# Kernel tuning notes

Measured on AMD Instinct MI355X. Metric: run time of the kernel, lower is better.

## Reference

```python
import jax, jax.numpy as jnp
import numpy as np

B, T, D = 16, 2048, 512
DB, K, TOPK, WIN = 128, 7, 16, 64
GATE_CAP = 0.5
STRAND_CAP = 0.5
_PHI = 1.618033988749895
_PSI = -0.6180339887498949


def _ln(x, w, b):
    mu = jnp.mean(x, -1, keepdims=True)
    var = jnp.var(x, -1, keepdims=True)
    return (x - mu) * jax.lax.rsqrt(var + 1e-5) * w + b


def setup_inputs() -> dict:
    key = jax.random.key(0)
    ks = jax.random.split(key, 20)
    def nrm(i, shape, scale=1.0):
        return jax.random.normal(ks[i], shape, dtype=jnp.float32) * jnp.float32(scale)
    return {
        'X_write': nrm(0, (B, T, D)),
        'X_read': nrm(1, (B, T, D)),
        'slots': nrm(2, (B, K, DB)),
        'W0': nrm(3, (D, D), D ** -0.5),
        'ln_write_w': jnp.ones((D,), jnp.float32),
        'ln_write_b': jnp.zeros((D,), jnp.float32),
        'W_V': nrm(4, (D, DB), D ** -0.5),
        'W_K_slot': nrm(5, (DB, DB), DB ** -0.5),
        'slot_key_bias': nrm(6, (K, DB), 2.0),
        'W_gate_w': nrm(7, (2 * DB, DB), (2 * DB) ** -0.5),
        'W_gate_b': jnp.full((DB,), -2.0, jnp.float32),
        'ln_strand_w': jnp.ones((DB,), jnp.float32),
        'ln_strand_b': jnp.zeros((DB,), jnp.float32),
        'Ws_Q': nrm(8, (DB, DB), DB ** -0.5),
        'Ws_K': nrm(9, (DB, DB), DB ** -0.5),
        'Ws_V': nrm(10, (DB, DB), DB ** -0.5),
        'lambda_strand': nrm(11, (DB,), 0.5),
        'W_Q_read': nrm(12, (D, DB), D ** -0.5),
        'W_K_read': nrm(13, (DB, DB), DB ** -0.5),
        'W_V_read': nrm(14, (DB, D), DB ** -0.5),
        'render_coeffs': nrm(15, (K, 3, D), 0.2),
        'slot_temps': jnp.ones((K,), jnp.float32),
    }


def _forward(X_write, X_read, slots, W0, ln_write_w, ln_write_b, W_V, W_K_slot,
             slot_key_bias, W_gate_w, W_gate_b, ln_strand_w, ln_strand_b,
             Ws_Q, Ws_K, Ws_V, lambda_strand, W_Q_read, W_K_read, W_V_read,
             render_coeffs, slot_temps):
    scale = jnp.float32(DB ** -0.5)
    W0_sg = jax.lax.stop_gradient(W0)
    X_n = _ln(X_write, ln_write_w, ln_write_b)

    # ---- windowed salience + topk pair selection (no-grad in original) ----
    X_nsg = jax.lax.stop_gradient(X_n)
    X_W0 = X_nsg @ W0_sg.T                      # [B,T,D]
    NEG = jnp.float32(-1e30)
    sal = []
    for o in range(1, WIN + 1):                 # offset j = i - o, fixed small loop
        s = jnp.sum(X_nsg[:, o:, :] * X_W0[:, :-o, :], axis=-1)  # [B, T-o]
        sal.append(jnp.pad(s, ((0, 0), (o, 0)), constant_values=NEG))
    sal = jnp.stack(sal, axis=-1).reshape(B, T * WIN)
    _, flat_idx = jax.lax.top_k(sal, TOPK)      # [B, TOPK]
    i_idx = flat_idx // WIN
    j_idx = i_idx - (flat_idx % WIN + 1)

    # ---- gather pairs, salience-weighted relation vector ----
    x_newer = jnp.take_along_axis(X_n, i_idx[:, :, None], axis=1)   # [B,TOPK,D]
    x_older = jnp.take_along_axis(X_n, j_idx[:, :, None], axis=1)
    pair_sal = jnp.sum(x_newer * (x_older @ W0_sg.T), axis=-1)      # [B,TOPK]
    alpha = jax.nn.softmax(pair_sal, axis=-1)
    rel = (x_newer - x_older) @ W_V                                 # [B,TOPK,DB]
    R_t = jnp.einsum('bk,bkd->bd', alpha, rel)                      # [B,DB]

    # ---- gated slot write ----
    slot_keys = slots @ W_K_slot + slot_key_bias                    # [B,K,DB]
    compat = jnp.einsum('bkd,bd->bk', slot_keys, R_t) * scale * jax.nn.softplus(slot_temps)
    sw = jax.nn.softmax(compat, axis=-1)
    weighted_R = sw[:, :, None] * R_t[:, None, :]                   # [B,K,DB]
    g = jax.nn.sigmoid(jnp.concatenate([slots, weighted_R], -1) @ W_gate_w + W_gate_b)
    slots_upd = (1.0 - g) * slots + g * weighted_R

    # ---- K x K strand mixer ----
    Bn = _ln(slots_upd, ln_strand_w, ln_strand_b)
    sa = jax.nn.softmax(jnp.einsum('bqd,bkd->bqk', Bn @ Ws_Q, Bn @ Ws_K) * scale, axis=-1)
    ctx = sa @ (Bn @ Ws_V)
    slots_next = slots_upd + ctx * jnp.clip(jnp.tanh(lambda_strand), -STRAND_CAP, STRAND_CAP)

    # ---- aux losses ----
    L_persist = jnp.mean((slots_next - slots) ** 2)
    nrm = jnp.maximum(jnp.linalg.norm(slots_next, axis=-1, keepdims=True), 1e-12)
    Bnorm = slots_next / nrm
    cos = jnp.einsum('bkd,bjd->bkj', Bnorm, Bnorm)
    off = ~jnp.eye(K, dtype=bool)
    L_div = jnp.mean((cos ** 2)[:, off])

    # ---- directional gated read attention ----
    q_r = X_read @ W_Q_read                                         # [B,T,DB]
    k_r = slots_next @ W_K_read                                     # [B,K,DB]
    v_r = slots_next @ W_V_read                                     # [B,K,D]
    scores = jnp.einsum('btd,bkd->btk', q_r, k_r) * scale
    q_mean = jnp.mean(X_read, axis=1)                               # [B,D]
    w0q = q_mean @ W0_sg.T
    denom = jnp.float32(_PHI - _PSI)
    phi_q = (w0q - _PSI * q_mean) / denom
    psi_q = (_PHI * q_mean - w0q) / denom
    phi_mag = jnp.linalg.norm(phi_q, axis=-1, keepdims=True)
    psi_mag = jnp.linalg.norm(psi_q, axis=-1, keepdims=True)
    total = phi_mag + psi_mag + 1e-6
    basis = jnp.concatenate([jnp.ones_like(phi_mag), phi_mag / total, psi_mag / total], -1)  # [B,3]
    gate = jnp.clip(jnp.tanh(jnp.einsum('bi,kid->bkd', basis, render_coeffs)), -GATE_CAP, GATE_CAP)
    z = jnp.einsum('btk,bkd->btd', jax.nn.softmax(scores, axis=-1), v_r * gate)
    return z, slots_next, L_persist, L_div


def reference(X_write, X_read, slots, W0, ln_write_w, ln_write_b, W_V, W_K_slot,
              slot_key_bias, W_gate_w, W_gate_b, ln_strand_w, ln_strand_b,
              Ws_Q, Ws_K, Ws_V, lambda_strand, W_Q_read, W_K_read, W_V_read,
              render_coeffs, slot_temps):
    return _forward(X_write, X_read, slots, W0, ln_write_w, ln_write_b, W_V, W_K_slot,
                    slot_key_bias, W_gate_w, W_gate_b, ln_strand_w, ln_strand_b,
                    Ws_Q, Ws_K, Ws_V, lambda_strand, W_Q_read, W_K_read, W_V_read,
                    render_coeffs, slot_temps)
```

## Files before the change

kernel.cpp:

```cpp
#include <hip/hip_runtime.h>
#include <math.h>

#define B_ 16
#define T_ 2048
#define D_ 512
#define DB_ 128
#define K_ 7
#define TOPK_ 16
#define WIN_ 64

static constexpr float SCALE_ = 0.08838834764831845f;
static constexpr float PHI_ = 1.618033988749895f;
static constexpr float PSI_ = -0.6180339887498949f;
static constexpr float INV_DENOM_ = 0.4472135954999579f;
static constexpr float NEGV = -1e30f;
static constexpr float NEGINF = -3.402823466e38f;
#define IMAXI 0x7FFFFFFF

typedef __attribute__((ext_vector_type(8))) __bf16 bf16x8;
typedef __attribute__((ext_vector_type(8))) unsigned short u16x8;
typedef __attribute__((ext_vector_type(4))) float f32x4;

__device__ inline float softplusf(float x){
    return fmaxf(x, 0.f) + log1pf(expf(-fabsf(x)));
// ... 84 lines not shown
        unsigned short h0 = f2bf(v.x), h1 = f2bf(v.y), h2 = f2bf(v.z), h3 = f2bf(v.w);
        ushort4 hv = make_ushort4(h0, h1, h2, h3);
        ushort4 lv = make_ushort4(f2bf(v.x - bf2f(h0)), f2bf(v.y - bf2f(h1)),
                                  f2bf(v.z - bf2f(h2)), f2bf(v.w - bf2f(h3)));
        *(ushort4*)&Wh[(size_t)gid*4] = hv;
        *(ushort4*)&Wl[(size_t)gid*4] = lv;
    } else {
        int idx = bx - 4352;
        int b_ = idx >> 5, c = idx & 31;
        const float* base = Xr + ((size_t)(b_*T_ + c*64)) * D_;
        float s0 = 0.f, s1 = 0.f;
        for (int t = 0; t < 64; t++) {
            s0 += base[(size_t)t*D_ + tid];
            s1 += base[(size_t)t*D_ + tid + 256];
        }
        qpart[((size_t)b_*32 + c)*D_ + tid] = s0;
        qpart[((size_t)b_*32 + c)*D_ + tid + 256] = s1;
    }
}

__global__ __launch_bounds__(256) void gemm_xw0_mfma(const unsigned short* __restrict__ Ah,
                                                     const unsigned short* __restrict__ Al,
                                                     const unsigned short* __restrict__ Wh,
                                                     const unsigned short* __restrict__ Wl,
                                                     float* __restrict__ Cf)
{
    __shared__ __align__(16) unsigned short sAh[2*128*32], sAl[2*128*32], sBh[2*128*32], sBl[2*128*32];
    int t0 = blockIdx.x * 128, d0 = blockIdx.y * 128;
    int tid = threadIdx.x;
    int lane = tid & 63, wid = tid >> 6;
    int wr = wid >> 1, wc = wid & 1;
    int fr = lane & 15;
    int kc2 = ((((lane >> 4) + (fr >> 1)) & 3) * 8);

    f32x4 acc[4][4];
    #pragma unroll
    for (int m = 0; m < 4; m++)
        #pragma unroll
        for (int n = 0; n < 4; n++) acc[m][n] = (f32x4){0.f,0.f,0.f,0.f};

    const unsigned short* gs = (wid==0) ? Ah : (wid==1) ? Al : (wid==2) ? Wh : Wl;
    unsigned short* lsA = (wid==0) ? sAh : (wid==1) ? sAl : (wid==2) ? sBh : sBl;
    int rowoff = (wid < 2) ? t0 : d0;
    int cch = ((lane & 3) - ((lane >> 3) & 3)) & 3;
    const unsigned short* gbase = gs + (size_t)(rowoff + (lane >> 2))*512 + cch*8;

    #pragma unroll
    for (int i = 0; i < 8; i++)
        gload16(gbase + (size_t)(16*i)*512 + 0, lsA + i*512);

    for (int t = 0; t < 16; t++) {
        int cur = t & 1;
        __syncthreads();
        if (t < 15) {
            unsigned short* ls = lsA + (cur^1)*(128*32);
            int kk = (t+1)*32;
            #pragma unroll
            for (int i = 0; i < 8; i++)
                gload16(gbase + (size_t)(16*i)*512 + kk, ls + i*512);
        }
        int bo = cur*(128*32);
        bf16x8 ahf[4], alf[4], bhf[4], blf[4];
        #pragma unroll
        for (int m = 0; m < 4; m++) {
            int r = bo + (wr*64 + m*16 + fr)*32 + kc2;
            ahf[m] = ld_bf8(&sAh[r]);
            alf[m] = ld_bf8(&sAl[r]);
        }
        #pragma unroll
        for (int n = 0; n < 4; n++) {
            int r = bo + (wc*64 + n*16 + fr)*32 + kc2;
            bhf[n] = ld_bf8(&sBh[r]);
            blf[n] = ld_bf8(&sBl[r]);
        }
        #pragma unroll
        for (int m = 0; m < 4; m++)
            #pragma unroll
            for (int n = 0; n < 4; n++) {
                acc[m][n] = __builtin_amdgcn_mfma_f32_16x16x32_bf16(bhf[n], ahf[m], acc[m][n], 0, 0, 0);
                acc[m][n] = __builtin_amdgcn_mfma_f32_16x16x32_bf16(bhf[n], alf[m], acc[m][n], 0, 0, 0);
                acc[m][n] = __builtin_amdgcn_mfma_f32_16x16x32_bf16(blf[n], ahf[m], acc[m][n], 0, 0, 0);
            }
    }

    #pragma unroll
    for (int m = 0; m < 4; m++) {
        int t = t0 + wr*64 + m*16 + fr;
        #pragma unroll
        for (int n = 0; n < 4; n++) {
            int dbase = d0 + wc*64 + n*16 + (lane >> 4)*4;
            *(f32x4*)&Cf[(size_t)t*512 + dbase] = acc[m][n];
        }
    }
}

__global__ __launch_bounds__(256) void sal_mfma(const unsigned short* __restrict__ Xh,
                                                const unsigned short* __restrict__ Xl,
                                                const float* __restrict__ Cf,
                                                float* __restrict__ sal)
{
    int b = blockIdx.x, i0 = blockIdx.y * 64;
    __shared__ __align__(16) unsigned short sAh[64*32], sAl[64*32], sBh[128*32], sBl[128*32];
    int tid = threadIdx.x;
    int lane = tid & 63, wcw = tid >> 6;
    int fr = lane & 15;
    int kc2 = ((((lane >> 4) + (fr >> 1)) & 3) * 8);

    const unsigned short* XhB = Xh + (size_t)b*T_*D_;
    const unsigned short* XlB = Xl + (size_t)b*T_*D_;
    const float* CfB = Cf + (size_t)b*T_*D_;

    f32x4 acc[4][2];
    #pragma unroll
    for (int m = 0; m < 4; m++) { acc[m][0] = (f32x4){0.f,0.f,0.f,0.f}; acc[m][1] = (f32x4){0.f,0.f,0.f,0.f}; }

    int ar = tid >> 2, ac = tid & 3;
    int aslot = (ac + (ar >> 1)) & 3;
    int brow = tid >> 1, bhh = tid & 1;
    int jrow = i0 - 64 + brow;

    uint4 rAh, rAl;
    float4 rB0[2], rB1[2];

    auto LOAD = [&](int kk){
        rAh = *(const uint4*)(XhB + (size_t)(i0 + ar)*512 + kk + ac*8);
        rAl = *(const uint4*)(XlB + (size_t)(i0 + ar)*512 + kk + ac*8);
        #pragma unroll
        for (int cc = 0; cc < 2; cc++) {
            int c = 2*bhh + cc;
            if (jrow >= 0) {
                const float* src = CfB + (size_t)jrow*512 + kk + c*8;
                rB0[cc] = *(const float4*)src;
                rB1[cc] = *(const float4*)(src + 4);
            } else {
                rB0[cc] = make_float4(0.f,0.f,0.f,0.f);
                rB1[cc] = make_float4(0.f,0.f,0.f,0.f);
            }
        }
    };
    auto WRITE = [&](){
        *(uint4*)&sAh[ar*32 + aslot*8] = rAh;
        *(uint4*)&sAl[ar*32 + aslot*8] = rAl;
        #pragma unroll
        for (int cc = 0; cc < 2; cc++) {
            int c = 2*bhh + cc;
            int slot = (c + (brow >> 1)) & 3;
            uint4 hv, lv;
            float4 v0 = rB0[cc], v1 = rB1[cc];
            unsigned int h01 = pkbf(v0.x, v0.y), h23 = pkbf(v0.z, v0.w);
            unsigned int h45 = pkbf(v1.x, v1.y), h67 = pkbf(v1.z, v1.w);
            float r0 = v0.x - __uint_as_float(h01 << 16);
            float r1 = v0.y - __uint_as_float(h01 & 0xFFFF0000u);
            float r2 = v0.z - __uint_as_float(h23 << 16);
            float r3 = v0.w - __uint_as_float(h23 & 0xFFFF0000u);
            float r4 = v1.x - __uint_as_float(h45 << 16);
            float r5 = v1.y - __uint_as_float(h45 & 0xFFFF0000u);
            float r6 = v1.z - __uint_as_float(h67 << 16);
            float r7 = v1.w - __uint_as_float(h67 & 0xFFFF0000u);
            hv.x = h01; hv.y = h23; hv.z = h45; hv.w = h67;
            lv.x = pkbf(r0, r1); lv.y = pkbf(r2, r3); lv.z = pkbf(r4, r5); lv.w = pkbf(r6, r7);
            *(uint4*)&sBh[brow*32 + slot*8] = hv;
            *(uint4*)&sBl[brow*32 + slot*8] = lv;
        }
    };

    LOAD(0);
    for (int t = 0; t < 16; t++) {
        WRITE();
        __syncthreads();
        int kkn = (t+1)*32;
        bf16x8 ahf[4], alf[4], bhf[2], blf[2];
        #pragma unroll
        for (int m = 0; m < 4; m++) {
            int r = (m*16 + fr)*32 + kc2;
            ahf[m] = ld_bf8(&sAh[r]);
            alf[m] = ld_bf8(&sAl[r]);
        }
        #pragma unroll
        for (int n = 0; n < 2; n++) {
            int r = (wcw*32 + n*16 + fr)*32 + kc2;
            bhf[n] = ld_bf8(&sBh[r]);
            blf[n] = ld_bf8(&sBl[r]);
        }
        if (t < 15) LOAD(kkn);
        #pragma unroll
        for (int m = 0; m < 4; m++)
            #pragma unroll
            for (int n = 0; n < 2; n++) {
                acc[m][n] = __builtin_amdgcn_mfma_f32_16x16x32_bf16(ahf[m], bhf[n], acc[m][n], 0, 0, 0);
                acc[m][n] = __builtin_amdgcn_mfma_f32_16x16x32_bf16(ahf[m], blf[n], acc[m][n], 0, 0, 0);
                acc[m][n] = __builtin_amdgcn_mfma_f32_16x16x32_bf16(alf[m], bhf[n], acc[m][n], 0, 0, 0);
            }
        __syncthreads();
    }

    float* salB = sal + (size_t)b*T_*WIN_;
    #pragma unroll
    for (int m = 0; m < 4; m++) {
        #pragma unroll
        for (int n = 0; n < 2; n++) {
            int jl = wcw*32 + n*16 + fr;
            #pragma unroll
            for (int r = 0; r < 4; r++) {
                int il = m*16 + (lane >> 4)*4 + r;
                int o = il - jl + 64;
                if (o >= 1 && o <= 64) {
                    int jg = i0 - 64 + jl;
                    salB[(size_t)(i0 + il)*WIN_ + (o - 1)] = (jg >= 0) ? acc[m][n][r] : NEGV;
                }
            }
        }
    }
}

__global__ __launch_bounds__(256) void topk_stage1(const float* __restrict__ sal,
                                                   float* __restrict__ cv, int* __restrict__ ci,
                                                   const float* __restrict__ qpart,
                                                   const float* __restrict__ W0,
                                                   float* __restrict__ w0p)
{
    int b = blockIdx.x, tid = threadIdx.x;
    if (blockIdx.y >= 64) {
        int c = blockIdx.y - 64;
        __shared__ float qm[D_];
        for (int p = tid; p < D_; p += 256) {
            float s = 0.f;
            for (int cc = 0; cc < 32; cc++) s += qpart[((size_t)b*32 + cc)*D_ + p];
            qm[p] = s * (1.f/2048.f);
        }
        __syncthreads();
        int w = tid >> 6, lane = tid & 63;
        float ph = 0.f, ps = 0.f;
        for (int r = 0; r < 16; r++) {
            int d = c*64 + w*16 + r;
            const float* wr = W0 + (size_t)d*D_;
            float s = 0.f;
            #pragma unroll
            for (int q = 0; q < 8; q++) s += qm[lane + q*64] * wr[lane + q*64];
            #pragma unroll
            for (int off = 32; off; off >>= 1) s += __shfl_xor(s, off);
            float phi = (s - PSI_*qm[d]) * INV_DENOM_;
            float psi = (PHI_*qm[d] - s) * INV_DENOM_;
            ph += phi*phi; ps += psi*psi;
        }
        __shared__ float shp[4], shs[4];
        if (lane == 0) { shp[w] = ph; shs[w] = ps; }
        __syncthreads();
        if (tid == 0) {
            w0p[((size_t)b*8 + c)*2 + 0] = shp[0]+shp[1]+shp[2]+shp[3];
            w0p[((size_t)b*8 + c)*2 + 1] = shs[0]+shs[1]+shs[2]+shs[3];
        }
        return;
    }
    int c = blockIdx.y;
    const float* s = sal + (size_t)b*(T_*WIN_) + (size_t)c*2048;
    int base = c*2048;
    int lane = tid & 63, wvi = tid >> 6;
    float v0=NEGINF,v1=NEGINF,v2=NEGINF,v3=NEGINF,v4=NEGINF,v5=NEGINF,v6=NEGINF,v7=NEGINF;
    int   i0=IMAXI, i1=IMAXI, i2=IMAXI, i3=IMAXI, i4=IMAXI, i5=IMAXI, i6=IMAXI, i7=IMAXI;
    #pragma unroll
    for (int r = 0; r < 8; r++) {
        int p = tid + r*256;
        float v = s[p];
        int idx = base + p;
        if (v > v7 || (v == v7 && idx < i7)) {
            bool b6 = (v > v6) || (v == v6 && idx < i6);
            bool b5 = (v > v5) || (v == v5 && idx < i5);
            bool b4 = (v > v4) || (v == v4 && idx < i4);
            bool b3 = (v > v3) || (v == v3 && idx < i3);
            bool b2 = (v > v2) || (v == v2 && idx < i2);
            bool b1 = (v > v1) || (v == v1 && idx < i1);
            bool b0 = (v > v0) || (v == v0 && idx < i0);
            float n7 = b6 ? v6 : v;             int m7 = b6 ? i6 : idx;
            float n6 = b6 ? (b5 ? v5 : v) : v6; int m6 = b6 ? (b5 ? i5 : idx) : i6;
            float n5 = b5 ? (b4 ? v4 : v) : v5; int m5 = b5 ? (b4 ? i4 : idx) : i5;
            float n4 = b4 ? (b3 ? v3 : v) : v4; int m4 = b4 ? (b3 ? i3 : idx) : i4;
            float n3 = b3 ? (b2 ? v2 : v) : v3; int m3 = b3 ? (b2 ? i2 : idx) : i3;
            float n2 = b2 ? (b1 ? v1 : v) : v2; int m2 = b2 ? (b1 ? i1 : idx) : i2;
            float n1 = b1 ? (b0 ? v0 : v) : v1; int m1 = b1 ? (b0 ? i0 : idx) : i1;
            float n0 = b0 ? v : v0;             int m0 = b0 ? idx : i0;
            v7=n7;i7=m7; v6=n6;i6=m6; v5=n5;i5=m5; v4=n4;i4=m4;
            v3=n3;i3=m3; v2=n2;i2=m2; v1=n1;i1=m1; v0=n0;i0=m0;
        }
    }
    float* cvo = cv + (((size_t)b*64 + c)*64) + wvi*16;
    int*   cio = ci + (((size_t)b*64 + c)*64) + wvi*16;
    for (int r = 0; r < 16; r++) {
        float bv = v0; int bi = i0;
        float wv_ = bv; int wi = bi;
        #pragma unroll
        for (int off = 1; off < 64; off <<= 1) {
            float vx = __shfl_xor(wv_, off);
            int   ix = __shfl_xor(wi, off);
            if (vx > wv_ || (vx == wv_ && ix < wi)) { wv_ = vx; wi = ix; }
        }
        if (bv == wv_ && bi == wi) {
            v0=v1;i0=i1; v1=v2;i1=i2; v2=v3;i2=i3; v3=v4;i3=i4;
            v4=v5;i4=i5; v5=v6;i5=i6; v6=v7;i6=i7; v7=NEGINF;i7=IMAXI;
        }
        if (lane == 0) { cvo[r] = wv_; cio[r] = wi; }
    }
}

__global__ __launch_bounds__(1024) void slot_kernel(
    const unsigned short* __restrict__ Xh, const unsigned short* __restrict__ Xl,
    const float* __restrict__ slots_in,
    const float* __restrict__ cv, const int* __restrict__ ci,
    const float* __restrict__ W_V, const float* __restrict__ W_K_slot, const float* __restrict__ skb,
    const float* __restrict__ Wg, const float* __restrict__ Wgb,
    const float* __restrict__ lnw, const float* __restrict__ lnb,
    const float* __restrict__ WsQ, const float* __restrict__ WsK, const float* __restrict__ WsV,
    const float* __restrict__ lambda_, const float* __restrict__ temps,
    float* __restrict__ snws, float* __restrict__ out_slots,
    float* __restrict__ lpP, float* __restrict__ lpD)
{
    int b = blockIdx.x, tid = threadIdx.x;
    int lane = tid & 63, wvi = tid >> 6;
    __shared__ float wbuf[128*DB_];
    __shared__ float alpha[16];
    __shared__ int   tis[16], tjs[16];
    __shared__ float tvv[16]; __shared__ int tii[16];
    __shared__ float scv[256]; __shared__ int sci[256];
    __shared__ float y[D_];
    __shared__ float part[8][DB_];
    __shared__ float pf[1024];
    __shared__ float Rt[DB_];
    __shared__ float sl[K_][DB_];
    __shared__ float upd[K_][DB_];
    __shared__ float Bn[K_][DB_];
    __shared__ float qq[K_][DB_], kk2[K_][DB_], vv[K_][DB_];
    __shared__ float snsh[K_][DB_];
    __shared__ float swv[K_], compat[K_], mu7[K_], rs7[K_], nr7[K_], ldv[K_];
    __shared__ float sa[K_][K_];

    auto STAGE = [&](const float* src){
        #pragma unroll
        for (int i = 0; i < 4; i++)
            ((float4*)wbuf)[tid + i*1024] = ((const float4*)src)[tid + i*1024];
    };

    for (int p = tid; p < K_*DB_; p += 1024) sl[p>>7][p&127] = slots_in[(size_t)b*K_*DB_ + p];

    {
        const float* cvb = cv + (size_t)b*4096;
        const int*   cib = ci + (size_t)b*4096;
        float v0=NEGINF,v1=NEGINF,v2=NEGINF,v3=NEGINF;
        int   i0=IMAXI, i1=IMAXI, i2=IMAXI, i3=IMAXI;
        #pragma unroll
        for (int r = 0; r < 4; r++) {
            int p = tid + r*1024;
            float v = cvb[p];
            int idx = cib[p];
            if (v > v3 || (v == v3 && idx < i3)) {
                bool b2 = (v > v2) || (v == v2 && idx < i2);
                bool b1 = (v > v1) || (v == v1 && idx < i1);
                bool b0 = (v > v0) || (v == v0 && idx < i0);
                float n3 = b2 ? v2 : v;             int m3 = b2 ? i2 : idx;
                float n2 = b2 ? (b1 ? v1 : v) : v2; int m2 = b2 ? (b1 ? i1 : idx) : i2;
                float n1 = b1 ? (b0 ? v0 : v) : v1; int m1 = b1 ? (b0 ? i0 : idx) : i1;
                float n0 = b0 ? v : v0;             int m0 = b0 ? idx : i0;
                v3=n3;i3=m3; v2=n2;i2=m2; v1=n1;i1=m1; v0=n0;i0=m0;
            }
        }
        for (int r = 0; r < 16; r++) {
            float bv = v0; int bi = i0;
            float wv_ = bv; int wi = bi;
            #pragma unroll
            for (int off = 1; off < 64; off <<= 1) {
                float vx = __shfl_xor(wv_, off);
                int   ix = __shfl_xor(wi, off);
                if (vx > wv_ || (vx == wv_ && ix < wi)) { wv_ = vx; wi = ix; }
            }
            if (bv == wv_ && bi == wi) {
                v0=v1;i0=i1; v1=v2;i1=i2; v2=v3;i2=i3; v3=NEGINF;i3=IMAXI;
            }
            if (lane == 0) { scv[wvi*16 + r] = wv_; sci[wvi*16 + r] = wi; }
        }
        __syncthreads();
        if (wvi == 0) {
            float u0=NEGINF,u1=NEGINF,u2=NEGINF,u3=NEGINF;
            int   j0=IMAXI, j1=IMAXI, j2=IMAXI, j3=IMAXI;
            #pragma unroll
            for (int r = 0; r < 4; r++) {
                int p = lane + r*64;
                float v = scv[p]; int idx = sci[p];
                if (v > u3 || (v == u3 && idx < j3)) {
                    bool b2 = (v > u2) || (v == u2 && idx < j2);
                    bool b1 = (v > u1) || (v == u1 && idx < j1);
                    bool b0 = (v > u0) || (v == u0 && idx < j0);
                    float n3 = b2 ? u2 : v;             int m3 = b2 ? j2 : idx;
                    float n2 = b2 ? (b1 ? u1 : v) : u2; int m2 = b2 ? (b1 ? j1 : idx) : j2;
                    float n1 = b1 ? (b0 ? u0 : v) : u1; int m1 = b1 ? (b0 ? j0 : idx) : j1;
                    float n0 = b0 ? v : u0;             int m0 = b0 ? idx : j0;
                    u3=n3;j3=m3; u2=n2;j2=m2; u1=n1;j1=m1; u0=n0;j0=m0;
                }
            }
            for (int r = 0; r < 16; r++) {
                float bv = u0; int bi = j0;
                float wv_ = bv; int wi = bi;
                #pragma unroll
                for (int off = 1; off < 64; off <<= 1) {
                    float vx = __shfl_xor(wv_, off);
                    int   ix = __shfl_xor(wi, off);
                    if (vx > wv_ || (vx == wv_ && ix < wi)) { wv_ = vx; wi = ix; }
                }
                if (bv == wv_ && bi == wi) {
                    u0=u1;j0=j1; u1=u2;j1=j2; u2=u3;j2=j3; u3=NEGINF;j3=IMAXI;
                }
                if (lane == 0) { tvv[r] = wv_; tii[r] = wi; }
            }
        }
        __syncthreads();
    }
    if (tid < 16) {
        float v = tvv[tid];
        int flat = tii[tid];
        tis[tid] = flat >> 6;
        tjs[tid] = (flat >> 6) - ((flat & 63) + 1);
        float m = v;
        #pragma unroll
        for (int off = 8; off; off >>= 1) m = fmaxf(m, __shfl_xor(m, off, 16));
        float e = expf(v - m);
        float s = e;
        #pragma unroll
        for (int off = 8; off; off >>= 1) s += __shfl_xor(s, off, 16);
        alpha[tid] = e / s;
    }
    __syncthreads();

    if (tid < D_) {
        float acc = 0.f;
        #pragma unroll
        for (int k = 0; k < 16; k++) {
            int i = tis[k], j = tjs[k];
            float xi = bf2f(Xh[((size_t)b*T_ + i)*D_ + tid]) + bf2f(Xl[((size_t)b*T_ + i)*D_ + tid]);
            float xj = bf2f(Xh[((size_t)b*T_ + j)*D_ + tid]) + bf2f(Xl[((size_t)b*T_ + j)*D_ + tid]);
            acc += alpha[k] * (xi - xj);
        }
        y[tid] = acc;
    }
    __syncthreads();

    {
        int g = tid >> 7, d = tid & 127;
        float rt_part = 0.f;
        for (int c = 0; c < 4; c++) {
            STAGE(W_V + (size_t)c*128*DB_);
            __syncthreads();
            int e0 = g*16;
            #pragma unroll
            for (int e = 0; e < 16; e++)
                rt_part += y[c*128 + e0 + e] * wbuf[(e0 + e)*DB_ + d];
            __syncthreads();
        }
        part[g][d] = rt_part;
    }
    __syncthreads();
    if (tid < DB_) {
        float acc = 0.f;
        #pragma unroll
        for (int g = 0; g < 8; g++) acc += part[g][tid];
        Rt[tid] = acc;
    }
    __syncthreads();

    STAGE(W_K_slot);
    __syncthreads();
    if (tid < K_*DB_) {
        int k = tid >> 7, d = tid & 127;
        float acc = skb[k*DB_ + d];
        #pragma unroll 8
        for (int e = 0; e < DB_; e++) acc += sl[k][e] * wbuf[e*DB_ + d];
        qq[k][d] = acc * Rt[d];
    }
    __syncthreads();
    if (wvi < K_) {
        float acc = qq[wvi][lane] + qq[wvi][lane + 64];
        #pragma unroll
        for (int off = 32; off; off >>= 1) acc += __shfl_xor(acc, off);
        if (lane == 0) compat[wvi] = acc * SCALE_ * softplusf(temps[wvi]);
    }
    __syncthreads();
    if (tid == 0) {
        float m = compat[0];
        for (int k = 1; k < K_; k++) m = fmaxf(m, compat[k]);
        float ssum = 0.f;
        for (int k = 0; k < K_; k++) { float e = expf(compat[k]-m); swv[k] = e; ssum += e; }
        for (int k = 0; k < K_; k++) swv[k] /= ssum;
    }
    __syncthreads();

    float gacc1 = 0.f;
    STAGE(Wg);
    __syncthreads();
    if (tid < K_*DB_) {
        int k = tid >> 7, d = tid & 127;
        #pragma unroll 8
        for (int e = 0; e < DB_; e++) gacc1 += sl[k][e] * wbuf[e*DB_ + d];
    }
    __syncthreads();
    STAGE(Wg + (size_t)DB_*DB_);
    __syncthreads();
    if (tid < K_*DB_) {
        int k = tid >> 7, d = tid & 127;
        float swk = swv[k];
        float acc = gacc1 + Wgb[d];
        #pragma unroll 8
        for (int e = 0; e < DB_; e++) acc += swk * Rt[e] * wbuf[e*DB_ + d];
        float g = 1.f / (1.f + expf(-acc));
        upd[k][d] = (1.f - g) * sl[k][d] + g * (swk * Rt[d]);
    }
    __syncthreads();

    if (wvi < K_) {
        float vv0 = upd[wvi][lane], vv1 = upd[wvi][lane + 64];
        float s = vv0 + vv1, ss = vv0*vv0 + vv1*vv1;
        #pragma unroll
        for (int off = 32; off; off >>= 1) { s += __shfl_xor(s, off); ss += __shfl_xor(ss, off); }
        if (lane == 0) {
            float mu = s / (float)DB_;
            mu7[wvi] = mu;
            rs7[wvi] = rsqrtf(ss/(float)DB_ - mu*mu + 1e-5f);
        }
    }
    __syncthreads();
    if (tid < K_*DB_) {
        int k = tid >> 7, d = tid & 127;
        Bn[k][d] = (upd[k][d] - mu7[k]) * rs7[k] * lnw[d] + lnb[d];
    }
    __syncthreads();

    STAGE(WsQ);
    __syncthreads();
    if (tid < K_*DB_) {
        int k = tid >> 7, d = tid & 127;
        float a = 0.f;
        #pragma unroll 8
        for (int e = 0; e < DB_; e++) a += Bn[k][e] * wbuf[e*DB_ + d];
        qq[k][d] = a;
    }
    __syncthreads();
    STAGE(WsK);
    __syncthreads();
    if (tid < K_*DB_) {
        int k = tid >> 7, d = tid & 127;
        float a = 0.f;
        #pragma unroll 8
        for (int e = 0; e < DB_; e++) a += Bn[k][e] * wbuf[e*DB_ + d];
        kk2[k][d] = a;
    }
    __syncthreads();
    STAGE(WsV);
    __syncthreads();
    if (tid < K_*DB_) {
        int k = tid >> 7, d = tid & 127;
        float a = 0.f;
        #pragma unroll 8
        for (int e = 0; e < DB_; e++) a += Bn[k][e] * wbuf[e*DB_ + d];
        vv[k][d] = a;
    }
    __syncthreads();

    if (wvi < K_) {
        int j = lane >> 3, s = lane & 7;
        float acc = 0.f;
        if (j < K_) {
            int e0 = s * 16;
            for (int e = e0; e < e0 + 16; e++) acc += qq[wvi][e] * kk2[j][e];
        }
        #pragma unroll
        for (int off = 4; off; off >>= 1) acc += __shfl_xor(acc, off, 8);
        if (s == 0 && j < K_) sa[wvi][j] = acc * SCALE_;
    }
    __syncthreads();
    if (tid < K_) {
        float m = sa[tid][0];
        for (int j = 1; j < K_; j++) m = fmaxf(m, sa[tid][j]);
        float ssum = 0.f;
        for (int j = 0; j < K_; j++) { float e = expf(sa[tid][j]-m); sa[tid][j] = e; ssum += e; }
        for (int j = 0; j < K_; j++) sa[tid][j] /= ssum;
    }
    __syncthreads();

    if (tid < K_*DB_) {
        int k = tid >> 7, d = tid & 127;
        float lam = tanhf(lambda_[d]);
        lam = fminf(fmaxf(lam, -0.5f), 0.5f);
        float c = 0.f;
        #pragma unroll
        for (int j = 0; j < K_; j++) c += sa[k][j] * vv[j][d];
        float sn = upd[k][d] + c * lam;
        snsh[k][d] = sn;
        snws[((size_t)b*K_ + k)*DB_ + d] = sn;
        out_slots[((size_t)b*K_ + k)*DB_ + d] = sn;
    }
    __syncthreads();

    {
        float dsq = 0.f;
        if (tid < K_*DB_) {
            int k = tid >> 7, d = tid & 127;
            float dd = snsh[k][d] - sl[k][d];
            dsq = dd*dd;
        }
        pf[tid] = dsq;
        if (wvi < K_) {
            float vv0 = snsh[wvi][lane], vv1 = snsh[wvi][lane + 64];
            float ss = vv0*vv0 + vv1*vv1;
            #pragma unroll
            for (int off = 32; off; off >>= 1) ss += __shfl_xor(ss, off);
            if (lane == 0) nr7[wvi] = fmaxf(sqrtf(ss), 1e-12f);
        }
        __syncthreads();
        if (wvi == 0) {
            float s = 0.f;
            #pragma unroll
            for (int q = 0; q < 16; q++) s += pf[lane + q*64];
            #pragma unroll
            for (int off = 32; off; off >>= 1) s += __shfl_xor(s, off);
            if (lane == 0) lpP[b] = s;
        }
        if (wvi >= 1 && wvi <= K_) {
            int q = wvi - 1;
            float accq = 0.f;
            for (int j = 0; j < K_; j++) {
                if (j == q) continue;
                float dt = snsh[q][lane]*snsh[j][lane] + snsh[q][lane+64]*snsh[j][lane+64];
                #pragma unroll
                for (int off = 32; off; off >>= 1) dt += __shfl_xor(dt, off);
                float cs = dt / (nr7[q] * nr7[j]);
                accq += cs*cs;
            }
            if (lane == 0) ldv[q] = accq;
        }
        __syncthreads();
        if (tid == 0) {
            float s = 0.f;
            for (int q = 0; q < K_; q++) s += ldv[q];
            lpD[b] = s;
        }
    }
}

__global__ __launch_bounds__(256) void kqvg_kernel(
    const float* __restrict__ sn, const float* __restrict__ WKr,
    const float* __restrict__ WQr, const float* __restrict__ WVr,
    const float* __restrict__ rc, const float* __restrict__ w0p,
    const float* __restrict__ lpP, const float* __restrict__ lpD,
    float* __restrict__ kq, float* __restrict__ vg, float* __restrict__ loss_out)
{
    int b = blockIdx.x, k = blockIdx.y, tid = threadIdx.x;
    if (b == 0 && k == 0 && tid == 0) {
        float s = 0.f, s2 = 0.f;
        for (int bb = 0; bb < B_; bb++) { s += lpP[bb]; s2 += lpD[bb]; }
        loss_out[0] = s / (float)(B_*K_*DB_);
        loss_out[1] = s2 / (float)(B_*(K_*K_-K_));
    }
    float P = 0.f, Q = 0.f;
    #pragma unroll
    for (int c = 0; c < 8; c++) {
        P += w0p[((size_t)b*8 + c)*2 + 0];
        Q += w0p[((size_t)b*8 + c)*2 + 1];
    }
    float pm = sqrtf(P), qm2 = sqrtf(Q);
    float tot = pm + qm2 + 1e-6f;
    float b1 = pm / tot, b2 = qm2 / tot;

    __shared__ float sl[DB_], kr[DB_];
    if (tid < DB_) sl[tid] = sn[((size_t)b*K_ + k)*DB_ + tid];
    __syncthreads();
    if (tid < DB_) {
        float a = 0.f;
        for (int e = 0; e < DB_; e++) a += sl[e] * WKr[(size_t)e*DB_ + tid];
        kr[tid] = a;
    }
    __syncthreads();
    #pragma unroll
    for (int rep = 0; rep < 2; rep++) {
        int e = tid + rep*256;
        float a = 0.f;
        const float* wq = WQr + (size_t)e*DB_;
        for (int d = 0; d < DB_; d++) a += kr[d] * wq[d];
        kq[((size_t)b*K_ + k)*D_ + e] = a;
    }
    #pragma unroll
    for (int rep = 0; rep < 2; rep++) {
        int dd = tid + rep*256;
        float a = 0.f;
        for (int e = 0; e < DB_; e++) a += sl[e] * WVr[(size_t)e*D_ + dd];
        float gpre = rc[((size_t)k*3 + 0)*D_ + dd] + b1*rc[((size_t)k*3 + 1)*D_ + dd] + b2*rc[((size_t)k*3 + 2)*D_ + dd];
        float g = tanhf(gpre);
        g = fminf(fmaxf(g, -0.5f), 0.5f);
        vg[((size_t)b*K_ + k)*D_ + dd] = a * g;
    }
}

__global__ __launch_bounds__(256) void z_kernel(const float* __restrict__ Xr,
                                                const float* __restrict__ kq,
                                                const float* __restrict__ vg,
                                                float* __restrict__ z)
{
    int b = blockIdx.x;
    int t0 = blockIdx.y * 64;
    __shared__ float kqs[K_][D_];
    __shared__ float vgs[K_][D_];
    int tid = threadIdx.x;
    for (int p = tid; p < K_*D_; p += 256) {
        kqs[p>>9][p&511] = kq[(size_t)b*K_*D_ + p];
        vgs[p>>9][p&511] = vg[(size_t)b*K_*D_ + p];
    }
    __syncthreads();
    int lane = tid & 63, w = tid >> 6;
    for (int it = 0; it < 16; it++) {
        int t = t0 + w*16 + it;
        const float* x = Xr + ((size_t)b*T_ + t)*D_;
        float xr[8];
        float s[K_] = {0,0,0,0,0,0,0};
        #pragma unroll
        for (int r = 0; r < 8; r++) {
            int e = lane + r*64;
            xr[r] = x[e];
            #pragma unroll
            for (int k = 0; k < K_; k++) s[k] += xr[r] * kqs[k][e];
        }
        #pragma unroll
        for (int k = 0; k < K_; k++)
            for (int off = 32; off; off >>= 1) s[k] += __shfl_xor(s[k], off);
        float sc[K_];
        float m = NEGINF;
        #pragma unroll
        for (int k = 0; k < K_; k++) { sc[k] = s[k] * SCALE_; m = fmaxf(m, sc[k]); }
        float p[K_], ssum = 0.f;
        #pragma unroll
        for (int k = 0; k < K_; k++) { p[k] = expf(sc[k] - m); ssum += p[k]; }
        float inv = 1.f / ssum;
        float* zp = z + ((size_t)b*T_ + t)*D_;
        #pragma unroll
        for (int r = 0; r < 8; r++) {
            int e = lane + r*64;
            float a = 0.f;
            #pragma unroll
            for (int k = 0; k < K_; k++) a += p[k] * vgs[k][e];
            zp[e] = a * inv;
        }
    }
}

extern "C" void kernel_launch(void* const* d_in, const int* in_sizes, int n_in,
                              void* d_out, int out_size, void* d_ws, size_t ws_size,
                              hipStream_t stream)
{
    const float* X_write = (const float*)d_in[0];
    const float* X_read  = (const float*)d_in[1];
    const float* slots   = (const float*)d_in[2];
    const float* W0      = (const float*)d_in[3];
    const float* lnw_w   = (const float*)d_in[4];
    const float* lnw_b   = (const float*)d_in[5];
    const float* W_V     = (const float*)d_in[6];
    const float* W_K_slot= (const float*)d_in[7];
    const float* skb     = (const float*)d_in[8];
    const float* Wg      = (const float*)d_in[9];
    const float* Wgb     = (const float*)d_in[10];
    const float* lns_w   = (const float*)d_in[11];
    const float* lns_b   = (const float*)d_in[12];
    const float* WsQ     = (const float*)d_in[13];
    const float* WsK     = (const float*)d_in[14];
    const float* WsV     = (const float*)d_in[15];
    const float* lambda_ = (const float*)d_in[16];
    const float* WQr     = (const float*)d_in[17];
    const float* WKr     = (const float*)d_in[18];
    const float* WVr     = (const float*)d_in[19];
    const float* rc      = (const float*)d_in[20];
    const float* temps   = (const float*)d_in[21];

    const size_t NXD = (size_t)B_*T_*D_;
    unsigned short* Xh  = (unsigned short*)d_ws;
    unsigned short* Xl  = Xh + NXD;
    float* Cf           = (float*)(Xl + NXD);
    unsigned short* W0h = (unsigned short*)(Cf + NXD);
    unsigned short* W0l = W0h + (size_t)D_*D_;
    float* fscr  = (float*)(W0l + (size_t)D_*D_);
    float* qpart = fscr;
    float* w0p   = qpart + (size_t)B_*32*D_;
    float* snws  = w0p + 256;
    float* kq    = snws + (size_t)B_*K_*DB_;
    float* vg    = kq + (size_t)B_*K_*D_;
    float* cv    = vg + (size_t)B_*K_*D_;
    int*   ci    = (int*)(cv + (size_t)B_*64*64);
    float* lpP   = (float*)(ci + (size_t)B_*64*64);
    float* lpD   = lpP + 16;

    float* z_out     = (float*)d_out;
    float* slots_out = z_out + NXD;
    float* loss_out  = slots_out + (size_t)B_*K_*DB_;
    float* sal       = z_out;

    prep_kernel<<<dim3(4096 + 256 + 512), dim3(256), 0, stream>>>(
        X_write, lnw_w, lnw_b, Xh, Xl, W0, W0h, W0l, X_read, qpart);
    gemm_xw0_mfma<<<dim3(B_*T_/128, D_/128), dim3(256), 0, stream>>>(Xh, Xl, W0h, W0l, Cf);
    sal_mfma<<<dim3(B_, T_/64), dim3(256), 0, stream>>>(Xh, Xl, Cf, sal);
    topk_stage1<<<dim3(B_, 72), dim3(256), 0, stream>>>(sal, cv, ci, qpart, W0, w0p);
    slot_kernel<<<dim3(B_), dim3(1024), 0, stream>>>(Xh, Xl, slots, cv, ci,
        W_V, W_K_slot, skb, Wg, Wgb, lns_w, lns_b, WsQ, WsK, WsV, lambda_, temps,
        snws, slots_out, lpP, lpD);
    kqvg_kernel<<<dim3(B_, K_), dim3(256), 0, stream>>>(snws, WKr, WQr, WVr, rc, w0p,
        lpP, lpD, kq, vg, loss_out);
    z_kernel<<<dim3(B_, T_/64), dim3(256), 0, stream>>>(X_read, kq, vg, z_out);
}
```

Before: 267.3 us.

## Split slot kernel into head, Rt-projection and double-buffered main kernels

The single 16-block slot kernel is split into three kernels. A 512-thread head kernel does the top-k selection and builds the weighted pair difference, a 128-block kernel computes the W_V projection in parallel, and the main kernel stages weight matrices in half-tiles with async global-to-LDS loads into a double buffer, so each load overlaps the previous tile's compute. The aim is to shorten the serial latency of the low-parallelism slot stage by spreading the W_V work and hiding weight staging. In exchange it adds two kernel launches and workspace round trips, and it relies on a gload16 helper that is not shown here.

```diff
diff --git a/kernel.cpp b/kernel.cpp
--- a/kernel.cpp
+++ b/kernel.cpp
@@ -410,11 +410,133 @@
     }
 }
 
-__global__ __launch_bounds__(1024) void slot_kernel(
+__global__ __launch_bounds__(512) void slot_head(
     const unsigned short* __restrict__ Xh, const unsigned short* __restrict__ Xl,
-    const float* __restrict__ slots_in,
     const float* __restrict__ cv, const int* __restrict__ ci,
-    const float* __restrict__ W_V, const float* __restrict__ W_K_slot, const float* __restrict__ skb,
+    float* __restrict__ yws)
+{
+    int b = blockIdx.x, tid = threadIdx.x;
+    int lane = tid & 63, wvi = tid >> 6;
+    __shared__ float scv[128]; __shared__ int sci[128];
+    __shared__ float tvv[16]; __shared__ int tii[16];
+    __shared__ float alpha[16]; __shared__ int tis[16], tjs[16];
+
+    const float* cvb = cv + (size_t)b*4096;
+    const int*   cib = ci + (size_t)b*4096;
+    float v0=NEGINF,v1=NEGINF,v2=NEGINF,v3=NEGINF,v4=NEGINF,v5=NEGINF,v6=NEGINF,v7=NEGINF;
+    int   i0=IMAXI, i1=IMAXI, i2=IMAXI, i3=IMAXI, i4=IMAXI, i5=IMAXI, i6=IMAXI, i7=IMAXI;
+    #pragma unroll
+    for (int r = 0; r < 8; r++) {
+        int p = tid + r*512;
+        float v = cvb[p];
+        int idx = cib[p];
+        if (v > v7 || (v == v7 && idx < i7)) {
+            bool b6 = (v > v6) || (v == v6 && idx < i6);
+            bool b5 = (v > v5) || (v == v5 && idx < i5);
+            bool b4 = (v > v4) || (v == v4 && idx < i4);
+            bool b3 = (v > v3) || (v == v3 && idx < i3);
+            bool b2 = (v > v2) || (v == v2 && idx < i2);
+            bool b1 = (v > v1) || (v == v1 && idx < i1);
+            bool b0 = (v > v0) || (v == v0 && idx < i0);
+            float n7 = b6 ? v6 : v;             int m7 = b6 ? i6 : idx;
+            float n6 = b6 ? (b5 ? v5 : v) : v6; int m6 = b6 ? (b5 ? i5 : idx) : i6;
+            float n5 = b5 ? (b4 ? v4 : v) : v5; int m5 = b5 ? (b4 ? i4 : idx) : i5;
+            float n4 = b4 ? (b3 ? v3 : v) : v4; int m4 = b4 ? (b3 ? i3 : idx) : i4;
+            float n3 = b3 ? (b2 ? v2 : v) : v3; int m3 = b3 ? (b2 ? i2 : idx) : i3;
+            float n2 = b2 ? (b1 ? v1 : v) : v2; int m2 = b2 ? (b1 ? i1 : idx) : i2;
+            float n1 = b1 ? (b0 ? v0 : v) : v1; int m1 = b1 ? (b0 ? i0 : idx) : i1;
+            float n0 = b0 ? v : v0;             int m0 = b0 ? idx : i0;
+            v7=n7;i7=m7; v6=n6;i6=m6; v5=n5;i5=m5; v4=n4;i4=m4;
+            v3=n3;i3=m3; v2=n2;i2=m2; v1=n1;i1=m1; v0=n0;i0=m0;
+        }
+    }
+    for (int r = 0; r < 16; r++) {
+        float bv = v0; int bi = i0;
+        float wv_ = bv; int wi = bi;
+        #pragma unroll
+        for (int off = 1; off < 64; off <<= 1) {
+            float vx = __shfl_xor(wv_, off);
+            int   ix = __shfl_xor(wi, off);
+            if (vx > wv_ || (vx == wv_ && ix < wi)) { wv_ = vx; wi = ix; }
+        }
+        if (bv == wv_ && bi == wi) {
+            v0=v1;i0=i1; v1=v2;i1=i2; v2=v3;i2=i3; v3=v4;i3=i4;
+            v4=v5;i4=i5; v5=v6;i5=i6; v6=v7;i6=i7; v7=NEGINF;i7=IMAXI;
+        }
+        if (lane == 0) { scv[wvi*16 + r] = wv_; sci[wvi*16 + r] = wi; }
+    }
+    __syncthreads();
+    if (wvi == 0) {
+        float a0 = scv[lane], a1 = scv[lane + 64];
+        int   e0 = sci[lane], e1 = sci[lane + 64];
+        bool sw = (a1 > a0) || (a1 == a0 && e1 < e0);
+        float u0 = sw ? a1 : a0; int j0 = sw ? e1 : e0;
+        float u1 = sw ? a0 : a1; int j1 = sw ? e0 : e1;
+        for (int r = 0; r < 16; r++) {
+            float bv = u0; int bi = j0;
+            float wv_ = bv; int wi = bi;
+            #pragma unroll
+            for (int off = 1; off < 64; off <<= 1) {
+                float vx = __shfl_xor(wv_, off);
+                int   ix = __shfl_xor(wi, off);
+                if (vx > wv_ || (vx == wv_ && ix < wi)) { wv_ = vx; wi = ix; }
+            }
+            if (bv == wv_ && bi == wi) { u0 = u1; j0 = j1; u1 = NEGINF; j1 = IMAXI; }
+            if (lane == 0) { tvv[r] = wv_; tii[r] = wi; }
+        }
+    }
+    __syncthreads();
+    if (tid < 16) {
+        float v = tvv[tid];
+        int flat = tii[tid];
+        tis[tid] = flat >> 6;
+        tjs[tid] = (flat >> 6) - ((flat & 63) + 1);
+        float m = v;
+        #pragma unroll
+        for (int off = 8; off; off >>= 1) m = fmaxf(m, __shfl_xor(m, off, 16));
+        float e = expf(v - m);
+        float s = e;
+        #pragma unroll
+        for (int off = 8; off; off >>= 1) s += __shfl_xor(s, off, 16);
+        alpha[tid] = e / s;
+    }
+    __syncthreads();
+    {
+        float acc = 0.f;
+        #pragma unroll
+        for (int k = 0; k < 16; k++) {
+            int i = tis[k], j = tjs[k];
+            float xi = bf2f(Xh[((size_t)b*T_ + i)*D_ + tid]) + bf2f(Xl[((size_t)b*T_ + i)*D_ + tid]);
+            float xj = bf2f(Xh[((size_t)b*T_ + j)*D_ + tid]) + bf2f(Xl[((size_t)b*T_ + j)*D_ + tid]);
+            acc += alpha[k] * (xi - xj);
+        }
+        yws[(size_t)b*D_ + tid] = acc;
+    }
+}
+
+__global__ __launch_bounds__(256) void slot_rt(const float* __restrict__ yws,
+                                               const float* __restrict__ W_V,
+                                               float* __restrict__ rtp)
+{
+    int b = blockIdx.x, c = blockIdx.y, tid = threadIdx.x;
+    __shared__ float ysl[64];
+    __shared__ float hsum[2][DB_];
+    if (tid < 64) ysl[tid] = yws[(size_t)b*D_ + c*64 + tid];
+    __syncthreads();
+    int d = tid & 127, h = tid >> 7;
+    float acc = 0.f;
+    int e0 = h*32;
+    #pragma unroll 8
+    for (int e = e0; e < e0 + 32; e++)
+        acc += ysl[e] * W_V[(size_t)(c*64 + e)*DB_ + d];
+    hsum[h][d] = acc;
+    __syncthreads();
+    if (tid < DB_) rtp[((size_t)b*8 + c)*DB_ + tid] = hsum[0][tid] + hsum[1][tid];
+}
+
+__global__ __launch_bounds__(1024) void slot_main(
+    const float* __restrict__ slots_in, const float* __restrict__ rtp,
+    const float* __restrict__ W_K_slot, const float* __restrict__ skb,
     const float* __restrict__ Wg, const float* __restrict__ Wgb,
     const float* __restrict__ lnw, const float* __restrict__ lnb,
     const float* __restrict__ WsQ, const float* __restrict__ WsK, const float* __restrict__ WsV,
@@ -424,162 +546,48 @@
 {
     int b = blockIdx.x, tid = threadIdx.x;
     int lane = tid & 63, wvi = tid >> 6;
-    __shared__ float wbuf[128*DB_];
-    __shared__ float alpha[16];
-    __shared__ int   tis[16], tjs[16];
-    __shared__ float tvv[16]; __shared__ int tii[16];
-    __shared__ float scv[256]; __shared__ int sci[256];
-    __shared__ float y[D_];
-    __shared__ float part[8][DB_];
-    __shared__ float pf[1024];
+    __shared__ __align__(16) float wbuf[2*8192];
     __shared__ float Rt[DB_];
     __shared__ float sl[K_][DB_];
     __shared__ float upd[K_][DB_];
     __shared__ float Bn[K_][DB_];
     __shared__ float qq[K_][DB_], kk2[K_][DB_], vv[K_][DB_];
     __shared__ float snsh[K_][DB_];
+    __shared__ float pf[1024];
     __shared__ float swv[K_], compat[K_], mu7[K_], rs7[K_], nr7[K_], ldv[K_];
     __shared__ float sa[K_][K_];
 
-    auto STAGE = [&](const float* src){
-        #pragma unroll
-        for (int i = 0; i < 4; i++)
-            ((float4*)wbuf)[tid + i*1024] = ((const float4*)src)[tid + i*1024];
+    auto ISSUE = [&](const float* src, int buf){
+        const float* g = src + (wvi*2)*256 + lane*4;
+        float* l = wbuf + buf*8192 + (wvi*2)*256;
+        gload16(g, l);
+        gload16(g + 256, l + 256);
     };
 
+    int kk_ = tid >> 7, dd_ = tid & 127;
+    bool act = tid < K_*DB_;
+
+    ISSUE(W_K_slot, 0);
     for (int p = tid; p < K_*DB_; p += 1024) sl[p>>7][p&127] = slots_in[(size_t)b*K_*DB_ + p];
-
-    {
-        const float* cvb = cv + (size_t)b*4096;
-        const int*   cib = ci + (size_t)b*4096;
-        float v0=NEGINF,v1=NEGINF,v2=NEGINF,v3=NEGINF;
-        int   i0=IMAXI, i1=IMAXI, i2=IMAXI, i3=IMAXI;
-        #pragma unroll
-        for (int r = 0; r < 4; r++) {
-            int p = tid + r*1024;
-            float v = cvb[p];
-            int idx = cib[p];
-            if (v > v3 || (v == v3 && idx < i3)) {
-                bool b2 = (v > v2) || (v == v2 && idx < i2);
-                bool b1 = (v > v1) || (v == v1 && idx < i1);
-                bool b0 = (v > v0) || (v == v0 && idx < i0);
-                float n3 = b2 ? v2 : v;             int m3 = b2 ? i2 : idx;
-                float n2 = b2 ? (b1 ? v1 : v) : v2; int m2 = b2 ? (b1 ? i1 : idx) : i2;
-                float n1 = b1 ? (b0 ? v0 : v) : v1; int m1 = b1 ? (b0 ? i0 : idx) : i1;
-                float n0 = b0 ? v : v0;             int m0 = b0 ? idx : i0;
-                v3=n3;i3=m3; v2=n2;i2=m2; v1=n1;i1=m1; v0=n0;i0=m0;
-            }
-        }
-        for (int r = 0; r < 16; r++) {
-            float bv = v0; int bi = i0;
-            float wv_ = bv; int wi = bi;
-            #pragma unroll
-            for (int off = 1; off < 64; off <<= 1) {
-                float vx = __shfl_xor(wv_, off);
-                int   ix = __shfl_xor(wi, off);
-                if (vx > wv_ || (vx == wv_ && ix < wi)) { wv_ = vx; wi = ix; }
-            }
-            if (bv == wv_ && bi == wi) {
-                v0=v1;i0=i1; v1=v2;i1=i2; v2=v3;i2=i3; v3=NEGINF;i3=IMAXI;
-            }
-            if (lane == 0) { scv[wvi*16 + r] = wv_; sci[wvi*16 + r] = wi; }
-        }
-        __syncthreads();
-        if (wvi == 0) {
-            float u0=NEGINF,u1=NEGINF,u2=NEGINF,u3=NEGINF;
-            int   j0=IMAXI, j1=IMAXI, j2=IMAXI, j3=IMAXI;
-            #pragma unroll
-            for (int r = 0; r < 4; r++) {
-                int p = lane + r*64;
-                float v = scv[p]; int idx = sci[p];
-                if (v > u3 || (v == u3 && idx < j3)) {
-                    bool b2 = (v > u2) || (v == u2 && idx < j2);
-                    bool b1 = (v > u1) || (v == u1 && idx < j1);
-                    bool b0 = (v > u0) || (v == u0 && idx < j0);
-                    float n3 = b2 ? u2 : v;             int m3 = b2 ? j2 : idx;
-                    float n2 = b2 ? (b1 ? u1 : v) : u2; int m2 = b2 ? (b1 ? j1 : idx) : j2;
-                    float n1 = b1 ? (b0 ? u0 : v) : u1; int m1 = b1 ? (b0 ? j0 : idx) : j1;
-                    float n0 = b0 ? v : u0;             int m0 = b0 ? idx : j0;
-                    u3=n3;j3=m3; u2=n2;j2=m2; u1=n1;j1=m1; u0=n0;j0=m0;
-                }
-            }
-            for (int r = 0; r < 16; r++) {
-                float bv = u0; int bi = j0;
-                float wv_ = bv; int wi = bi;
-                #pragma unroll
-                for (int off = 1; off < 64; off <<= 1) {
-                    float vx = __shfl_xor(wv_, off);
-                    int   ix = __shfl_xor(wi, off);
-                    if (vx > wv_ || (vx == wv_ && ix < wi)) { wv_ = vx; wi = ix; }
-                }
-                if (bv == wv_ && bi == wi) {
-                    u0=u1;j0=j1; u1=u2;j1=j2; u2=u3;j2=j3; u3=NEGINF;j3=IMAXI;
-                }
-                if (lane == 0) { tvv[r] = wv_; tii[r] = wi; }
-            }
-        }
-        __syncthreads();
-    }
-    if (tid < 16) {
-        float v = tvv[tid];
-        int flat = tii[tid];
-        tis[tid] = flat >> 6;
-        tjs[tid] = (flat >> 6) - ((flat & 63) + 1);
-        float m = v;
-        #pragma unroll
-        for (int off = 8; off; off >>= 1) m = fmaxf(m, __shfl_xor(m, off, 16));
-        float e = expf(v - m);
-        float s = e;
-        #pragma unroll
-        for (int off = 8; off; off >>= 1) s += __shfl_xor(s, off, 16);
-        alpha[tid] = e / s;
-    }
-    __syncthreads();
-
-    if (tid < D_) {
-        float acc = 0.f;
-        #pragma unroll
-        for (int k = 0; k < 16; k++) {
-            int i = tis[k], j = tjs[k];
-            float xi = bf2f(Xh[((size_t)b*T_ + i)*D_ + tid]) + bf2f(Xl[((size_t)b*T_ + i)*D_ + tid]);
-            float xj = bf2f(Xh[((size_t)b*T_ + j)*D_ + tid]) + bf2f(Xl[((size_t)b*T_ + j)*D_ + tid]);
-            acc += alpha[k] * (xi - xj);
-        }
-        y[tid] = acc;
-    }
-    __syncthreads();
-
-    {
-        int g = tid >> 7, d = tid & 127;
-        float rt_part = 0.f;
-        for (int c = 0; c < 4; c++) {
-            STAGE(W_V + (size_t)c*128*DB_);
-            __syncthreads();
-            int e0 = g*16;
-            #pragma unroll
-            for (int e = 0; e < 16; e++)
-                rt_part += y[c*128 + e0 + e] * wbuf[(e0 + e)*DB_ + d];
-            __syncthreads();
-        }
-        part[g][d] = rt_part;
-    }
-    __syncthreads();
     if (tid < DB_) {
-        float acc = 0.f;
-        #pragma unroll
-        for (int g = 0; g < 8; g++) acc += part[g][tid];
-        Rt[tid] = acc;
-    }
-    __syncthreads();
-
-    STAGE(W_K_slot);
-    __syncthreads();
-    if (tid < K_*DB_) {
-        int k = tid >> 7, d = tid & 127;
-        float acc = skb[k*DB_ + d];
-        #pragma unroll 8
-        for (int e = 0; e < DB_; e++) acc += sl[k][e] * wbuf[e*DB_ + d];
-        qq[k][d] = acc * Rt[d];
+        float a = 0.f;
+        #pragma unroll
+        for (int c = 0; c < 8; c++) a += rtp[((size_t)b*8 + c)*DB_ + tid];
+        Rt[tid] = a;
+    }
+    __syncthreads();
+    ISSUE(W_K_slot + 8192, 1);
+    float kacc = 0.f;
+    if (act) {
+        #pragma unroll 8
+        for (int e = 0; e < 64; e++) kacc += sl[kk_][e] * wbuf[e*DB_ + dd_];
+    }
+    __syncthreads();
+    ISSUE(Wg, 0);
+    if (act) {
+        #pragma unroll 8
+        for (int e = 0; e < 64; e++) kacc += sl[kk_][64+e] * wbuf[8192 + e*DB_ + dd_];
+        qq[kk_][dd_] = (kacc + skb[kk_*DB_ + dd_]) * Rt[dd_];
     }
     __syncthreads();
     if (wvi < K_) {
@@ -597,32 +605,38 @@
         for (int k = 0; k < K_; k++) swv[k] /= ssum;
     }
     __syncthreads();
-
-    float gacc1 = 0.f;
-    STAGE(Wg);
-    __syncthreads();
-    if (tid < K_*DB_) {
-        int k = tid >> 7, d = tid & 127;
-        #pragma unroll 8
-        for (int e = 0; e < DB_; e++) gacc1 += sl[k][e] * wbuf[e*DB_ + d];
-    }
-    __syncthreads();
-    STAGE(Wg + (size_t)DB_*DB_);
-    __syncthreads();
-    if (tid < K_*DB_) {
-        int k = tid >> 7, d = tid & 127;
-        float swk = swv[k];
-        float acc = gacc1 + Wgb[d];
-        #pragma unroll 8
-        for (int e = 0; e < DB_; e++) acc += swk * Rt[e] * wbuf[e*DB_ + d];
-        float g = 1.f / (1.f + expf(-acc));
-        upd[k][d] = (1.f - g) * sl[k][d] + g * (swk * Rt[d]);
-    }
-    __syncthreads();
-
+    ISSUE(Wg + 8192, 1);
+    float gacc = 0.f;
+    if (act) {
+        #pragma unroll 8
+        for (int e = 0; e < 64; e++) gacc += sl[kk_][e] * wbuf[e*DB_ + dd_];
+    }
+    __syncthreads();
+    ISSUE(Wg + 16384, 0);
+    if (act) {
+        #pragma unroll 8
+        for (int e = 0; e < 64; e++) gacc += sl[kk_][64+e] * wbuf[8192 + e*DB_ + dd_];
+    }
+    __syncthreads();
+    ISSUE(Wg + 24576, 1);
+    float g2acc = 0.f;
+    if (act) {
+        #pragma unroll 8
+        for (int e = 0; e < 64; e++) g2acc += Rt[e] * wbuf[e*DB_ + dd_];
+    }
+    __syncthreads();
+    ISSUE(WsQ, 0);
+    if (act) {
+        #pragma unroll 8
+        for (int e = 0; e < 64; e++) g2acc += Rt[64+e] * wbuf[8192 + e*DB_ + dd_];
+        float pre = gacc + swv[kk_]*g2acc + Wgb[dd_];
+        float g = 1.f / (1.f + expf(-pre));
+        upd[kk_][dd_] = (1.f - g) * sl[kk_][dd_] + g * (swv[kk_] * Rt[dd_]);
+    }
+    __syncthreads();
     if (wvi < K_) {
-        float vv0 = upd[wvi][lane], vv1 = upd[wvi][lane + 64];
-        float s = vv0 + vv1, ss = vv0*vv0 + vv1*vv1;
+        float a0 = upd[wvi][lane], a1 = upd[wvi][lane + 64];
+        float s = a0 + a1, ss = a0*a0 + a1*a1;
         #pragma unroll
         for (int off = 32; off; off >>= 1) { s += __shfl_xor(s, off); ss += __shfl_xor(ss, off); }
         if (lane == 0) {
@@ -632,40 +646,47 @@
         }
     }
     __syncthreads();
-    if (tid < K_*DB_) {
-        int k = tid >> 7, d = tid & 127;
-        Bn[k][d] = (upd[k][d] - mu7[k]) * rs7[k] * lnw[d] + lnb[d];
-    }
-    __syncthreads();
-
-    STAGE(WsQ);
-    __syncthreads();
-    if (tid < K_*DB_) {
-        int k = tid >> 7, d = tid & 127;
-        float a = 0.f;
-        #pragma unroll 8
-        for (int e = 0; e < DB_; e++) a += Bn[k][e] * wbuf[e*DB_ + d];
-        qq[k][d] = a;
-    }
-    __syncthreads();
-    STAGE(WsK);
-    __syncthreads();
-    if (tid < K_*DB_) {
-        int k = tid >> 7, d = tid & 127;
-        float a = 0.f;
-        #pragma unroll 8
-        for (int e = 0; e < DB_; e++) a += Bn[k][e] * wbuf[e*DB_ + d];
-        kk2[k][d] = a;
-    }
-    __syncthreads();
-    STAGE(WsV);
-    __syncthreads();
-    if (tid < K_*DB_) {
-        int k = tid >> 7, d = tid & 127;
-        float a = 0.f;
-        #pragma unroll 8
-        for (int e = 0; e < DB_; e++) a += Bn[k][e] * wbuf[e*DB_ + d];
-        vv[k][d] = a;
+    if (act) Bn[kk_][dd_] = (upd[kk_][dd_] - mu7[kk_]) * rs7[kk_] * lnw[dd_] + lnb[dd_];
+    __syncthreads();
+    ISSUE(WsQ + 8192, 1);
+    float qacc = 0.f;
+    if (act) {
+        #pragma unroll 8
+        for (int e = 0; e < 64; e++) qacc += Bn[kk_][e] * wbuf[e*DB_ + dd_];
+    }
+    __syncthreads();
+    ISSUE(WsK, 0);
+    if (act) {
+        #pragma unroll 8
+        for (int e = 0; e < 64; e++) qacc += Bn[kk_][64+e] * wbuf[8192 + e*DB_ + dd_];
+        qq[kk_][dd_] = qacc;
+    }
+    __syncthreads();
+    ISSUE(WsK + 8192, 1);
+    float kacc2 = 0.f;
+    if (act) {
+        #pragma unroll 8
+        for (int e = 0; e < 64; e++) kacc2 += Bn[kk_][e] * wbuf[e*DB_ + dd_];
+    }
+    __syncthreads();
+    ISSUE(WsV, 0);
+    if (act) {
+        #pragma unroll 8
+        for (int e = 0; e < 64; e++) kacc2 += Bn[kk_][64+e] * wbuf[8192 + e*DB_ + dd_];
+        kk2[kk_][dd_] = kacc2;
+    }
+    __syncthreads();
+    ISSUE(WsV + 8192, 1);
+    float vacc = 0.f;
+    if (act) {
+        #pragma unroll 8
+        for (int e = 0; e < 64; e++) vacc += Bn[kk_][e] * wbuf[e*DB_ + dd_];
+    }
+    __syncthreads();
+    if (act) {
+        #pragma unroll 8
+        for (int e = 0; e < 64; e++) vacc += Bn[kk_][64+e] * wbuf[8192 + e*DB_ + dd_];
+        vv[kk_][dd_] = vacc;
     }
     __syncthreads();
 
@@ -689,32 +710,25 @@
         for (int j = 0; j < K_; j++) sa[tid][j] /= ssum;
     }
     __syncthreads();
-
-    if (tid < K_*DB_) {
-        int k = tid >> 7, d = tid & 127;
-        float lam = tanhf(lambda_[d]);
+    if (act) {
+        float lam = tanhf(lambda_[dd_]);
         lam = fminf(fmaxf(lam, -0.5f), 0.5f);
         float c = 0.f;
         #pragma unroll
-        for (int j = 0; j < K_; j++) c += sa[k][j] * vv[j][d];
-        float sn = upd[k][d] + c * lam;
-        snsh[k][d] = sn;
-        snws[((size_t)b*K_ + k)*DB_ + d] = sn;
-        out_slots[((size_t)b*K_ + k)*DB_ + d] = sn;
-    }
-    __syncthreads();
-
+        for (int j = 0; j < K_; j++) c += sa[kk_][j] * vv[j][dd_];
+        float sn = upd[kk_][dd_] + c * lam;
+        snsh[kk_][dd_] = sn;
+        snws[((size_t)b*K_ + kk_)*DB_ + dd_] = sn;
+        out_slots[((size_t)b*K_ + kk_)*DB_ + dd_] = sn;
+    }
+    __syncthreads();
     {
         float dsq = 0.f;
-        if (tid < K_*DB_) {
-            int k = tid >> 7, d = tid & 127;
-            float dd = snsh[k][d] - sl[k][d];
-            dsq = dd*dd;
-        }
+        if (act) { float dd2 = snsh[kk_][dd_] - sl[kk_][dd_]; dsq = dd2*dd2; }
         pf[tid] = dsq;
         if (wvi < K_) {
-            float vv0 = snsh[wvi][lane], vv1 = snsh[wvi][lane + 64];
-            float ss = vv0*vv0 + vv1*vv1;
+            float a0 = snsh[wvi][lane], a1 = snsh[wvi][lane + 64];
+            float ss = a0*a0 + a1*a1;
             #pragma unroll
             for (int off = 32; off; off >>= 1) ss += __shfl_xor(ss, off);
             if (lane == 0) nr7[wvi] = fmaxf(sqrtf(ss), 1e-12f);
@@ -897,6 +911,8 @@
     int*   ci    = (int*)(cv + (size_t)B_*64*64);
     float* lpP   = (float*)(ci + (size_t)B_*64*64);
     float* lpD   = lpP + 16;
+    float* yws   = lpD + 16;
+    float* rtp   = yws + (size_t)B_*D_;
 
     float* z_out     = (float*)d_out;
     float* slots_out = z_out + NXD;
@@ -908,8 +924,10 @@
     gemm_xw0_mfma<<<dim3(B_*T_/128, D_/128), dim3(256), 0, stream>>>(Xh, Xl, W0h, W0l, Cf);
     sal_mfma<<<dim3(B_, T_/64), dim3(256), 0, stream>>>(Xh, Xl, Cf, sal);
     topk_stage1<<<dim3(B_, 72), dim3(256), 0, stream>>>(sal, cv, ci, qpart, W0, w0p);
-    slot_kernel<<<dim3(B_), dim3(1024), 0, stream>>>(Xh, Xl, slots, cv, ci,
-        W_V, W_K_slot, skb, Wg, Wgb, lns_w, lns_b, WsQ, WsK, WsV, lambda_, temps,
+    slot_head<<<dim3(B_), dim3(512), 0, stream>>>(Xh, Xl, cv, ci, yws);
+    slot_rt<<<dim3(B_, 8), dim3(256), 0, stream>>>(yws, W_V, rtp);
+    slot_main<<<dim3(B_), dim3(1024), 0, stream>>>(slots, rtp,
+        W_K_slot, skb, Wg, Wgb, lns_w, lns_b, WsQ, WsK, WsV, lambda_, temps,
         snws, slots_out, lpP, lpD);
     kqvg_kernel<<<dim3(B_, K_), dim3(256), 0, stream>>>(snws, WKr, WQr, WVr, rc, w0p,
         lpP, lpD, kq, vg, loss_out);
```

Result: no change. 265.5 us (-0.6%).
